# Performance work log

Hardware: AMD Instinct MI355X
Metric: run time of the kernel (lower is better)

Reference implementation:

```python
import jax, jax.numpy as jnp
from jax import lax
import numpy as np

SEQ_LEN, BATCH, NUM_TAGS = 512, 256, 128


def setup_inputs() -> dict:
    key = jax.random.key(0)
    k1, k2, k3, k4, k5 = jax.random.split(key, 5)
    emissions = jax.random.normal(k1, (SEQ_LEN, BATCH, NUM_TAGS), dtype=jnp.float32)
    tags = jax.random.randint(k2, (SEQ_LEN, BATCH), 0, NUM_TAGS, dtype=jnp.int64)
    mask = jnp.ones((SEQ_LEN, BATCH), dtype=bool)
    # CRF learned parameters (torchcrf initializes Uniform(-0.1, 0.1))
    start_transitions = jax.random.uniform(k3, (NUM_TAGS,), jnp.float32, -0.1, 0.1)
    end_transitions = jax.random.uniform(k4, (NUM_TAGS,), jnp.float32, -0.1, 0.1)
    transitions = jax.random.uniform(k5, (NUM_TAGS, NUM_TAGS), jnp.float32, -0.1, 0.1)
    return {
        "emissions": emissions,
        "tags": tags,
        "mask": mask,
        "start_transitions": start_transitions,
        "end_transitions": end_transitions,
        "transitions": transitions,
    }


def reference(emissions, tags, mask, start_transitions, end_transitions, transitions):
    """torchcrf CRF.forward(emissions, tags, mask, reduction='sum'):
    summed log-likelihood = numerator (gold path score) - log partition.
    emissions: [T, B, K], tags: [T, B], mask: [T, B] bool.
    """
    T, B = tags.shape
    maskf = mask.astype(emissions.dtype)
    bidx = jnp.arange(B)

    # ---- numerator: score of the gold tag sequence ----
    first_score = start_transitions[tags[0]] + emissions[0, bidx, tags[0]]  # [B]

    def num_step(carry, inp):
        score, prev_tags = carry
        em_t, tag_t, m_t = inp  # [B,K], [B], [B] float
        step = transitions[prev_tags, tag_t] + em_t[bidx, tag_t]
        score = score + step * m_t
        prev_tags = jnp.where(m_t.astype(bool), tag_t, prev_tags)
        return (score, prev_tags), None

    (num, last_tags), _ = lax.scan(
        num_step, (first_score, tags[0]), (emissions[1:], tags[1:], maskf[1:])
    )
    num = num + end_transitions[last_tags]  # [B]

    # ---- denominator: log partition via forward algorithm ----
    init = start_transitions[None, :] + emissions[0]  # [B, K]

    def den_step(score, inp):
        em_t, m_t = inp  # [B,K], [B] bool
        # broadcast: [B, K_prev, K_next]
        nxt = jax.nn.logsumexp(
            score[:, :, None] + transitions[None, :, :] + em_t[:, None, :], axis=1
        )
        score = jnp.where(m_t[:, None], nxt, score)
        return score, None

    final, _ = lax.scan(den_step, init, (emissions[1:], mask[1:]))
    den = jax.nn.logsumexp(final + end_transitions[None, :], axis=1)  # [B]

    # reduction='sum'
    return jnp.sum(num - den)
```

## Files before the change

### kernel.cpp

```cpp
#include <hip/hip_runtime.h>
#include <hip/hip_bf16.h>


#define TT 512
#define BB 256
#define KK 128
#define TB 32768

typedef float f2 __attribute__((ext_vector_type(2)));

#if __has_builtin(__builtin_elementwise_fma)
#define FMA2(a, b, c) __builtin_elementwise_fma((a), (b), (c))
#else
static __device__ __forceinline__ f2 FMA2(f2 a, f2 b, f2 c) {
  f2 r; r.x = fmaf(a.x, b.x, c.x); r.y = fmaf(a.y, b.y, c.y); return r;
}
#endif

#define HOT_BARRIER()                                    \
  do {                                                   \
    asm volatile("s_waitcnt lgkmcnt(0)" ::: "memory");   \
    __builtin_amdgcn_s_barrier();                        \
    asm volatile("" ::: "memory");                       \
  } while (0)

__global__ __launch_bounds__(512) void crf_main(
    const float* __restrict__ em,
    const int* __restrict__ tags_raw,
    const unsigned char* __restrict__ mask_raw,
    const float* __restrict__ startt,
    const float* __restrict__ endt,
    const float* __restrict__ trans,
    double* __restrict__ acc)
{
  const int b = blockIdx.x;
  const int tid = threadIdx.x;
  const int j = tid >> 2;
  const int q = tid & 3;
  const int wid = tid >> 6;
  const int qown = j >> 5;

  __shared__ __align__(16) float srep[2][144];
  __shared__ __align__(16) float wavesum[16];
  __shared__ int sflags[4];
  __shared__ unsigned char smask[TT];

  {
    int wv = (tid < 64) ? tags_raw[2 * tid + 1] : 0;
    unsigned long long bal = __ballot(wv != 0);
    if (tid == 0) {
      sflags[0] = (bal == 0ull) ? 1 : 0;
      sflags[1] = (mask_raw[1] != 0) ? 0 : 1;
    }
  }
  __syncthreads();
  const bool tags64 = (sflags[0] != 0);
  const bool mask32 = (sflags[1] != 0);
  const int* mask_i = (const int*)mask_raw;

  auto get_tag = [&](int t) -> int {
    int idx = t * BB + b;
    return tags64 ? tags_raw[2 * idx] : tags_raw[idx];
  };

  {
    int idx = tid * BB + b;
    bool m = mask32 ? (mask_i[idx] != 0) : (mask_raw[idx] != 0);
    smask[tid] = m ? 1 : 0;
  }
  __syncthreads();

  float ncon = 0.f, mcnt = 0.f;
  {
    const int t = tid;
    int ct = get_tag(t);
    bool m = (smask[t] != 0);
    if (m) mcnt = 1.f;
    if (t == 0) {
      ncon = startt[ct] + em[(size_t)b * KK + ct];
    } else if (m) {
      int pt = get_tag(t - 1);
      ncon = trans[pt * KK + ct] + em[((size_t)t * BB + b) * KK + ct];
    }
  }
  #pragma unroll
  for (int mm = 1; mm < 64; mm <<= 1) {
    ncon += __shfl_xor(ncon, mm, 64);
    mcnt += __shfl_xor(mcnt, mm, 64);
  }
  if ((tid & 63) == 0) {
    wavesum[wid] = ncon;
    wavesum[8 + wid] = mcnt;
  }
  __syncthreads();
  float num_b = 0.f;
  if (tid == 0) {
    float ns = 0.f, ms = 0.f;
    #pragma unroll
    for (int wv = 0; wv < 8; ++wv) { ns += wavesum[wv]; ms += wavesum[8 + wv]; }
    int L = (int)(ms + 0.5f);
    num_b = ns + endt[get_tag(L - 1)];
    sflags[2] = L;
  }

  const int bi = q * 32;
  f2 cl0, ch0, cl1, ch1, cl2, ch2, cl3, ch3, cl4, ch4, cl5, ch5, cl6, ch6, cl7, ch7;
  {
    const float* tp0 = trans + (size_t)bi * KK + j;
#define INITC(n)                                        \
    cl##n.x = __expf(tp0[(4 * n + 0) * KK]);            \
    cl##n.y = __expf(tp0[(4 * n + 1) * KK]);            \
    ch##n.x = __expf(tp0[(4 * n + 2) * KK]);            \
    ch##n.y = __expf(tp0[(4 * n + 3) * KK]);
    INITC(0) INITC(1) INITC(2) INITC(3) INITC(4) INITC(5) INITC(6) INITC(7)
#undef INITC
  }

  const float* emb = em + (size_t)b * KK + j;
  float e0 = __expf(startt[j] + emb[0]);
  if (q == qown) srep[0][j + 4 * qown] = e0;

  float pex = __expf(emb[(size_t)1 * TB]);
  float e1 = emb[(size_t)2 * TB];
  float e2 = emb[(size_t)3 * TB];
  float e3 = emb[(size_t)4 * TB];
  float e4 = emb[(size_t)5 * TB];
  float e5 = emb[(size_t)6 * TB];
  __syncthreads();
  const int L = sflags[2];

  int cur = 0;
  double Cacc = 0.0;

  for (int t = 1; t < L; ++t) {
    float ecur = pex;
    pex = __expf(e1);
    e1 = e2; e2 = e3; e3 = e4; e4 = e5;
    int tp = t + 6; if (tp > TT - 1) tp = TT - 1;
    e5 = emb[(size_t)tp * TB];

    const float4* sp = reinterpret_cast<const float4*>(&srep[cur][q * 36]);
    f2 a01 = {0.f, 0.f}, a23 = {0.f, 0.f};
#define DOT(n)                                           \
    { float4 s4 = sp[n];                                 \
      f2 slo = {s4.x, s4.y}; f2 shi = {s4.z, s4.w};      \
      a01 = FMA2(slo, cl##n, a01);                       \
      a23 = FMA2(shi, ch##n, a23); }
    DOT(0) DOT(1) DOT(2) DOT(3) DOT(4) DOT(5) DOT(6) DOT(7)
#undef DOT
    float v = (a01.x + a23.x) + (a01.y + a23.y);
    v += __shfl_xor(v, 1, 64);
    v += __shfl_xor(v, 2, 64);
    float w = v * ecur;

    if ((t & 3) == 1 && t != 1) {
      float4 wa = *reinterpret_cast<const float4*>(&wavesum[0]);
      float4 wb = *reinterpret_cast<const float4*>(&wavesum[4]);
      float tot = ((wa.x + wa.y) + (wa.z + wa.w)) + ((wb.x + wb.y) + (wb.z + wb.w));
      if (tid == 0) Cacc += (double)__logf(tot);
      w *= __builtin_amdgcn_rcpf(tot);
    }
    if (q == qown) srep[cur ^ 1][j + 4 * qown] = w;
    if ((t & 3) == 0) {
      float r = w;
      r += __shfl_xor(r, 4, 64);
      r += __shfl_xor(r, 8, 64);
      r += __shfl_xor(r, 16, 64);
      r += __shfl_xor(r, 32, 64);
      if ((tid & 63) == 0) wavesum[wid] = r;
    }
    HOT_BARRIER();
    cur ^= 1;
  }

  float x = srep[cur][j + 4 * qown] * __expf(endt[j]);
  x += __shfl_xor(x, 4, 64);
  x += __shfl_xor(x, 8, 64);
  x += __shfl_xor(x, 16, 64);
  x += __shfl_xor(x, 32, 64);
  if ((tid & 63) == 0) wavesum[wid] = x;
  __syncthreads();
  if (tid == 0) {
    float tot = 0.f;
    #pragma unroll
    for (int wv = 0; wv < 8; ++wv) tot += wavesum[wv];
    double den = Cacc + (double)__logf(tot);
    atomicAdd(acc, (double)num_b - den);
  }
}

__global__ void crf_finalize(const double* __restrict__ acc, float* __restrict__ out) {
  out[0] = (float)acc[0];
}

extern "C" void kernel_launch(void* const* d_in, const int* in_sizes, int n_in,
                              void* d_out, int out_size, void* d_ws, size_t ws_size,
                              hipStream_t stream) {
  const float* em    = (const float*)d_in[0];
  const int*   tags  = (const int*)d_in[1];
  const unsigned char* mask = (const unsigned char*)d_in[2];
  const float* startt = (const float*)d_in[3];
  const float* endt   = (const float*)d_in[4];
  const float* trans  = (const float*)d_in[5];
  double* acc = (double*)d_ws;

  hipMemsetAsync(d_ws, 0, sizeof(double), stream);
  crf_main<<<256, 512, 0, stream>>>(em, tags, mask, startt, endt, trans, acc);
  crf_finalize<<<1, 1, 0, stream>>>(acc, (float*)d_out);
}
```

Baseline: 326.3 us.

## Halve block size: each thread computes two output tags with packed FMAs

The block shrinks from 512 to 256 threads, and each thread now owns two adjacent next-tags instead of one, holding 32 packed transition-exponential pairs in registers. The per-step dot product uses broadcast packed FMAs, and the 4-lane reduction uses DPP instead of shuffles. Fewer waves take part in each per-timestep barrier, which is meant to lower sync latency on the serial recurrence. In exchange, each thread carries more register pressure and more FMA work per step. The rescaling sum is adjusted to four waves, including the 0.25 factor for the replicated lanes.

```diff
diff --git a/kernel.cpp b/kernel.cpp
--- a/kernel.cpp
+++ b/kernel.cpp
@@ -16,6 +16,14 @@
   f2 r; r.x = fmaf(a.x, b.x, c.x); r.y = fmaf(a.y, b.y, c.y); return r;
 }
 #endif
+
+static __device__ __forceinline__ float qsum4(float x) {
+  x += __int_as_float(__builtin_amdgcn_update_dpp(
+      0, __float_as_int(x), 0xB1, 0xF, 0xF, false));
+  x += __int_as_float(__builtin_amdgcn_update_dpp(
+      0, __float_as_int(x), 0x4E, 0xF, 0xF, false));
+  return x;
+}
 
 #define HOT_BARRIER()                                    \
   do {                                                   \
@@ -24,7 +32,7 @@
     asm volatile("" ::: "memory");                       \
   } while (0)
 
-__global__ __launch_bounds__(512) void crf_main(
+__global__ __launch_bounds__(256, 1) void crf_main(
     const float* __restrict__ em,
     const int* __restrict__ tags_raw,
     const unsigned char* __restrict__ mask_raw,
@@ -35,10 +43,10 @@
 {
   const int b = blockIdx.x;
   const int tid = threadIdx.x;
-  const int j = tid >> 2;
-  const int q = tid & 3;
+  const int jp = tid >> 2;
+  const int o = tid & 3;
   const int wid = tid >> 6;
-  const int qown = j >> 5;
+  const int woff = 36 * (jp >> 4) + 2 * (jp & 15);
 
   __shared__ __align__(16) float srep[2][144];
   __shared__ __align__(16) float wavesum[16];
@@ -63,24 +71,23 @@
     return tags64 ? tags_raw[2 * idx] : tags_raw[idx];
   };
 
-  {
-    int idx = tid * BB + b;
+  for (int t = tid; t < TT; t += 256) {
+    int idx = t * BB + b;
     bool m = mask32 ? (mask_i[idx] != 0) : (mask_raw[idx] != 0);
-    smask[tid] = m ? 1 : 0;
+    smask[t] = m ? 1 : 0;
   }
   __syncthreads();
 
   float ncon = 0.f, mcnt = 0.f;
-  {
-    const int t = tid;
+  for (int t = tid; t < TT; t += 256) {
     int ct = get_tag(t);
     bool m = (smask[t] != 0);
-    if (m) mcnt = 1.f;
+    if (m) mcnt += 1.f;
     if (t == 0) {
-      ncon = startt[ct] + em[(size_t)b * KK + ct];
+      ncon += startt[ct] + em[(size_t)b * KK + ct];
     } else if (m) {
       int pt = get_tag(t - 1);
-      ncon = trans[pt * KK + ct] + em[((size_t)t * BB + b) * KK + ct];
+      ncon += trans[pt * KK + ct] + em[((size_t)t * BB + b) * KK + ct];
     }
   }
   #pragma unroll
@@ -97,35 +104,52 @@
   if (tid == 0) {
     float ns = 0.f, ms = 0.f;
     #pragma unroll
-    for (int wv = 0; wv < 8; ++wv) { ns += wavesum[wv]; ms += wavesum[8 + wv]; }
+    for (int wv = 0; wv < 4; ++wv) { ns += wavesum[wv]; ms += wavesum[8 + wv]; }
     int L = (int)(ms + 0.5f);
     num_b = ns + endt[get_tag(L - 1)];
     sflags[2] = L;
   }
 
-  const int bi = q * 32;
-  f2 cl0, ch0, cl1, ch1, cl2, ch2, cl3, ch3, cl4, ch4, cl5, ch5, cl6, ch6, cl7, ch7;
-  {
-    const float* tp0 = trans + (size_t)bi * KK + j;
-#define INITC(n)                                        \
-    cl##n.x = __expf(tp0[(4 * n + 0) * KK]);            \
-    cl##n.y = __expf(tp0[(4 * n + 1) * KK]);            \
-    ch##n.x = __expf(tp0[(4 * n + 2) * KK]);            \
-    ch##n.y = __expf(tp0[(4 * n + 3) * KK]);
-    INITC(0) INITC(1) INITC(2) INITC(3) INITC(4) INITC(5) INITC(6) INITC(7)
+  f2 c0,  c1,  c2,  c3,  c4,  c5,  c6,  c7,
+     c8,  c9,  c10, c11, c12, c13, c14, c15,
+     c16, c17, c18, c19, c20, c21, c22, c23,
+     c24, c25, c26, c27, c28, c29, c30, c31;
+  {
+    const float* tp0 = trans + (size_t)(o * 32) * KK + 2 * jp;
+#define INITC(n)                                            \
+    { float2 tv = *(const float2*)(tp0 + (n) * KK);         \
+      c##n.x = __expf(tv.x); c##n.y = __expf(tv.y); }
+    INITC(0)  INITC(1)  INITC(2)  INITC(3)  INITC(4)  INITC(5)  INITC(6)  INITC(7)
+    INITC(8)  INITC(9)  INITC(10) INITC(11) INITC(12) INITC(13) INITC(14) INITC(15)
+    INITC(16) INITC(17) INITC(18) INITC(19) INITC(20) INITC(21) INITC(22) INITC(23)
+    INITC(24) INITC(25) INITC(26) INITC(27) INITC(28) INITC(29) INITC(30) INITC(31)
 #undef INITC
   }
-
-  const float* emb = em + (size_t)b * KK + j;
-  float e0 = __expf(startt[j] + emb[0]);
-  if (q == qown) srep[0][j + 4 * qown] = e0;
-
-  float pex = __expf(emb[(size_t)1 * TB]);
-  float e1 = emb[(size_t)2 * TB];
-  float e2 = emb[(size_t)3 * TB];
-  float e3 = emb[(size_t)4 * TB];
-  float e4 = emb[(size_t)5 * TB];
-  float e5 = emb[(size_t)6 * TB];
+  asm volatile("" : "+v"(c0),  "+v"(c1),  "+v"(c2),  "+v"(c3),
+                    "+v"(c4),  "+v"(c5),  "+v"(c6),  "+v"(c7),
+                    "+v"(c8),  "+v"(c9),  "+v"(c10), "+v"(c11),
+                    "+v"(c12), "+v"(c13), "+v"(c14), "+v"(c15));
+  asm volatile("" : "+v"(c16), "+v"(c17), "+v"(c18), "+v"(c19),
+                    "+v"(c20), "+v"(c21), "+v"(c22), "+v"(c23),
+                    "+v"(c24), "+v"(c25), "+v"(c26), "+v"(c27),
+                    "+v"(c28), "+v"(c29), "+v"(c30), "+v"(c31));
+
+  const float* emb = em + (size_t)b * KK + 2 * jp;
+  {
+    float2 st = *(const float2*)(startt + 2 * jp);
+    float2 e0 = *(const float2*)(emb);
+    if (o == 0) {
+      float2 s0 = {__expf(st.x + e0.x), __expf(st.y + e0.y)};
+      *(float2*)&srep[0][woff] = s0;
+    }
+  }
+
+  float2 er = *(const float2*)(emb + (size_t)1 * TB);
+  f2 pex; pex.x = __expf(er.x); pex.y = __expf(er.y);
+  float2 e1 = *(const float2*)(emb + (size_t)2 * TB);
+  float2 e2 = *(const float2*)(emb + (size_t)3 * TB);
+  float2 e3 = *(const float2*)(emb + (size_t)4 * TB);
+  float2 e4 = *(const float2*)(emb + (size_t)5 * TB);
   __syncthreads();
   const int L = sflags[2];
 
@@ -133,36 +157,47 @@
   double Cacc = 0.0;
 
   for (int t = 1; t < L; ++t) {
-    float ecur = pex;
-    pex = __expf(e1);
-    e1 = e2; e2 = e3; e3 = e4; e4 = e5;
-    int tp = t + 6; if (tp > TT - 1) tp = TT - 1;
-    e5 = emb[(size_t)tp * TB];
-
-    const float4* sp = reinterpret_cast<const float4*>(&srep[cur][q * 36]);
-    f2 a01 = {0.f, 0.f}, a23 = {0.f, 0.f};
-#define DOT(n)                                           \
-    { float4 s4 = sp[n];                                 \
-      f2 slo = {s4.x, s4.y}; f2 shi = {s4.z, s4.w};      \
-      a01 = FMA2(slo, cl##n, a01);                       \
-      a23 = FMA2(shi, ch##n, a23); }
-    DOT(0) DOT(1) DOT(2) DOT(3) DOT(4) DOT(5) DOT(6) DOT(7)
-#undef DOT
-    float v = (a01.x + a23.x) + (a01.y + a23.y);
-    v += __shfl_xor(v, 1, 64);
-    v += __shfl_xor(v, 2, 64);
-    float w = v * ecur;
+    f2 ecur = pex;
+    pex.x = __expf(e1.x); pex.y = __expf(e1.y);
+    e1 = e2; e2 = e3; e3 = e4;
+    int tp = t + 5; if (tp > TT - 1) tp = TT - 1;
+    e4 = *(const float2*)(emb + (size_t)tp * TB);
+
+    const float4* sp = reinterpret_cast<const float4*>(&srep[cur][o * 36]);
+    f2 a0 = {0.f, 0.f}, a1 = {0.f, 0.f}, a2 = {0.f, 0.f}, a3 = {0.f, 0.f};
+#define DOTQ(m, cA, cB, cC, cD, accA, accB)              \
+    { float4 s4 = sp[m];                                 \
+      f2 v0 = {s4.x, s4.x}, v1 = {s4.y, s4.y};           \
+      f2 v2 = {s4.z, s4.z}, v3 = {s4.w, s4.w};           \
+      accA = FMA2(v0, cA, accA); accB = FMA2(v1, cB, accB); \
+      accA = FMA2(v2, cC, accA); accB = FMA2(v3, cD, accB); }
+    DOTQ(0, c0,  c1,  c2,  c3,  a0, a1)
+    DOTQ(1, c4,  c5,  c6,  c7,  a2, a3)
+    DOTQ(2, c8,  c9,  c10, c11, a0, a1)
+    DOTQ(3, c12, c13, c14, c15, a2, a3)
+    DOTQ(4, c16, c17, c18, c19, a0, a1)
+    DOTQ(5, c20, c21, c22, c23, a2, a3)
+    DOTQ(6, c24, c25, c26, c27, a0, a1)
+    DOTQ(7, c28, c29, c30, c31, a2, a3)
+#undef DOTQ
+    f2 av = (a0 + a1) + (a2 + a3);
+    f2 w;
+    w.x = qsum4(av.x) * ecur.x;
+    w.y = qsum4(av.y) * ecur.y;
 
     if ((t & 3) == 1 && t != 1) {
       float4 wa = *reinterpret_cast<const float4*>(&wavesum[0]);
-      float4 wb = *reinterpret_cast<const float4*>(&wavesum[4]);
-      float tot = ((wa.x + wa.y) + (wa.z + wa.w)) + ((wb.x + wb.y) + (wb.z + wb.w));
+      float tot = 0.25f * ((wa.x + wa.y) + (wa.z + wa.w));
       if (tid == 0) Cacc += (double)__logf(tot);
-      w *= __builtin_amdgcn_rcpf(tot);
-    }
-    if (q == qown) srep[cur ^ 1][j + 4 * qown] = w;
+      float rt = __builtin_amdgcn_rcpf(tot);
+      w.x *= rt; w.y *= rt;
+    }
+    if (o == 0) {
+      float2 ws = {w.x, w.y};
+      *(float2*)&srep[cur ^ 1][woff] = ws;
+    }
     if ((t & 3) == 0) {
-      float r = w;
+      float r = w.x + w.y;
       r += __shfl_xor(r, 4, 64);
       r += __shfl_xor(r, 8, 64);
       r += __shfl_xor(r, 16, 64);
@@ -173,17 +208,19 @@
     cur ^= 1;
   }
 
-  float x = srep[cur][j + 4 * qown] * __expf(endt[j]);
-  x += __shfl_xor(x, 4, 64);
-  x += __shfl_xor(x, 8, 64);
-  x += __shfl_xor(x, 16, 64);
-  x += __shfl_xor(x, 32, 64);
-  if ((tid & 63) == 0) wavesum[wid] = x;
+  {
+    float2 sv = *(const float2*)&srep[cur][woff];
+    float2 ed = *(const float2*)(endt + 2 * jp);
+    float x = sv.x * __expf(ed.x) + sv.y * __expf(ed.y);
+    x += __shfl_xor(x, 4, 64);
+    x += __shfl_xor(x, 8, 64);
+    x += __shfl_xor(x, 16, 64);
+    x += __shfl_xor(x, 32, 64);
+    if ((tid & 63) == 0) wavesum[wid] = x;
+  }
   __syncthreads();
   if (tid == 0) {
-    float tot = 0.f;
-    #pragma unroll
-    for (int wv = 0; wv < 8; ++wv) tot += wavesum[wv];
+    float tot = 0.25f * (wavesum[0] + wavesum[1] + wavesum[2] + wavesum[3]);
     double den = Cacc + (double)__logf(tot);
     atomicAdd(acc, (double)num_b - den);
   }
@@ -205,6 +242,6 @@
   double* acc = (double*)d_ws;
 
   hipMemsetAsync(d_ws, 0, sizeof(double), stream);
-  crf_main<<<256, 512, 0, stream>>>(em, tags, mask, startt, endt, trans, acc);
+  crf_main<<<256, 256, 0, stream>>>(em, tags, mask, startt, endt, trans, acc);
   crf_finalize<<<1, 1, 0, stream>>>(acc, (float*)d_out);
 }
```

Result: faster. 316.6 us (-3.0%).
